# Kernel optimization log

Hardware: AMD Instinct MI355X
Metric: run time of the kernel (lower is better)

## Reference

```python
import jax, jax.numpy as jnp
import numpy as np

NUM_GRAPHS = 128
N_NODES = 50000
N_EDGES = 400000
EMB = 384
L = 5
BN_EPS = 1e-5


def _bn(h, gamma, beta):
    # training-mode BatchNorm1d over the node/edge dim (biased variance, like torch)
    m = h.mean(axis=0)
    v = h.var(axis=0)
    return gamma * (h - m) * jax.lax.rsqrt(v + BN_EPS) + beta


def setup_inputs() -> dict:
    key = jax.random.key(0)
    ks = jax.random.split(key, 16)
    batch = jnp.sort(jax.random.randint(ks[0], (N_NODES,), 0, NUM_GRAPHS))
    x = jax.random.randint(ks[1], (N_NODES, 9), 0, 64)
    edge_index = jax.random.randint(ks[2], (2, N_EDGES), 0, N_NODES)
    edge_attr = jax.random.randint(ks[3], (N_EDGES, 3), 0, 8)
    s = 0.05
    atom_emb = jax.random.normal(ks[4], (9, 64, EMB), jnp.float32) * s
    bond_emb = jax.random.normal(ks[5], (3, 8, EMB), jnp.float32) * s
    # per-layer GINE MLP params, stacked over layers
    W1 = jax.random.normal(ks[6], (L, EMB, 2 * EMB), jnp.float32) * (1.0 / np.sqrt(EMB))
    b1 = jnp.zeros((L, 2 * EMB), jnp.float32)
    g1 = jnp.ones((L, 2 * EMB), jnp.float32)
    be1 = jnp.zeros((L, 2 * EMB), jnp.float32)
    W2 = jax.random.normal(ks[7], (L, 2 * EMB, EMB), jnp.float32) * (1.0 / np.sqrt(2 * EMB))
    b2 = jnp.zeros((L, EMB), jnp.float32)
    # outer per-layer BatchNorm params
    gbn = jnp.ones((L, EMB), jnp.float32)
    bbn = jnp.zeros((L, EMB), jnp.float32)
    return {"batch": batch, "x": x, "edge_index": edge_index, "edge_attr": edge_attr,
            "atom_emb": atom_emb, "bond_emb": bond_emb,
            "W1": W1, "b1": b1, "g1": g1, "be1": be1,
            "W2": W2, "b2": b2, "gbn": gbn, "bbn": bbn}


def reference(batch, x, edge_index, edge_attr, atom_emb, bond_emb,
              W1, b1, g1, be1, W2, b2, gbn, bbn):
    # AtomEncoder / BondEncoder: sum of per-column embedding lookups
    h = atom_emb[jnp.arange(9), x].sum(axis=1)          # [N, EMB]
    e = bond_emb[jnp.arange(3), edge_attr].sum(axis=1)  # [E, EMB]
    src, dst = edge_index[0], edge_index[1]
    for i in range(W1.shape[0]):
        # GINEConv: sum_j relu(x_j + e_ij)  (edge_weight defaults to ones)
        msg = jax.nn.relu(h[src] + e)                                   # [E, EMB]
        agg = jax.ops.segment_sum(msg, dst, num_segments=N_NODES)      # [N, EMB]
        z = h + agg                                                     # (1+eps)*x_i + agg, eps=0
        # MLP: Linear -> BN -> ReLU -> Linear
        z = z @ W1[i] + b1[i]
        z = jax.nn.relu(_bn(z, g1[i], be1[i]))
        z = z @ W2[i] + b2[i]
        # outer BN + ReLU (drop_ratio = 0.0)
        h = jax.nn.relu(_bn(z, gbn[i], bbn[i]))
    # standard pooling: global_add_pool
    graph_emb = jax.ops.segment_sum(h, batch, num_segments=NUM_GRAPHS)  # [G, EMB]
    return graph_emb, h
```

## Files before the change

### kernel.cpp

```cpp
#include <hip/hip_runtime.h>
#include <stdint.h>

#define NN 50000
#define NE 400000
#define EMB 384
#define NH 768
#define NL 5

typedef __bf16 bf16x8_t __attribute__((ext_vector_type(8)));
typedef float  f32x4_t  __attribute__((ext_vector_type(4)));

__device__ __forceinline__ float bflo(uint32_t u){ union{uint32_t u;float f;} v; v.u = u<<16; return v.f; }
__device__ __forceinline__ float bfhi(uint32_t u){ union{uint32_t u;float f;} v; v.u = u & 0xffff0000u; return v.f; }
__device__ __forceinline__ uint16_t f2bf(float f){
  union{float f;uint32_t u;} v; v.f=f;
  uint32_t r = v.u + 0x7fffu + ((v.u>>16)&1u);
  return (uint16_t)(r>>16);
}
__device__ __forceinline__ uint32_t bfpack2(float a, float b){
  return (uint32_t)f2bf(a) | ((uint32_t)f2bf(b)<<16);
}

__device__ __forceinline__ void gld16(uint16_t* ldsp, const uint16_t* gp){
  __builtin_amdgcn_global_load_lds(
      (const __attribute__((address_space(1))) uint32_t*)gp,
      (__attribute__((address_space(3))) uint32_t*)ldsp,
      16, 0, 0);
}

__global__ void hist_kernel(const int* __restrict__ dst, int* __restrict__ count){
  int i = blockIdx.x*256 + threadIdx.x;
  if (i < NE) atomicAdd(&count[dst[i]], 1);
}
__global__ void scan_block_sum(const int* __restrict__ count, int* __restrict__ bsum, int n){
  __shared__ int s[256];
  int i = blockIdx.x*256 + threadIdx.x;
  s[threadIdx.x] = (i<n) ? count[i] : 0;
  __syncthreads();
  for (int st=128; st>0; st>>=1){
    if (threadIdx.x < st) s[threadIdx.x] += s[threadIdx.x+st];
    __syncthreads();
  }
  if (threadIdx.x==0) bsum[blockIdx.x] = s[0];
}
__global__ void scan_excl_small(int* __restrict__ bsum, int nb){
  __shared__ int s[256];
  int t = threadIdx.x;
  int v = (t<nb) ? bsum[t] : 0;
  s[t] = v;
  __syncthreads();
  for (int st=1; st<256; st<<=1){
    int u = (t>=st) ? s[t-st] : 0;
    __syncthreads();
    s[t] += u;
    __syncthreads();
  }
  if (t<nb) bsum[t] = s[t] - v;
}
__global__ void scan_final(const int* __restrict__ count, const int* __restrict__ bsum,
                           int* __restrict__ rowptr, int* __restrict__ cursor, int n){
  __shared__ int s[256];
  int t = threadIdx.x;
  int i = blockIdx.x*256 + t;
  int v = (i<n) ? count[i] : 0;
  s[t] = v;
  __syncthreads();
  for (int st=1; st<256; st<<=1){
    int u = (t>=st) ? s[t-st] : 0;
    __syncthreads();
    s[t] += u;
    __syncthreads();
  }
  int off = bsum[blockIdx.x] + s[t] - v;
  if (i < n){
    rowptr[i] = off; cursor[i] = off;
    if (i == n-1) rowptr[n] = off + v;
  }
}
__global__ void scatter_kernel(const int* __restrict__ dst, const int* __restrict__ src,
                               const int* __restrict__ eattr, int* __restrict__ cursor,
                               int* __restrict__ csr_src, int* __restrict__ csr_code){
  int e = blockIdx.x*256 + threadIdx.x;
  if (e < NE){
    int p = atomicAdd(&cursor[dst[e]], 1);
    csr_src[p] = src[e];
    csr_code[p] = eattr[e*3] | (eattr[e*3+1]<<3) | (eattr[e*3+2]<<6);
  }
}

__global__ void build_bond(const float* __restrict__ bemb, uint16_t* __restrict__ bt){
  const int code = blockIdx.x;
  const int t0 = code&7, t1=(code>>3)&7, t2=code>>6;
  const int c = threadIdx.x;
  const float2 a = ((const float2*)(bemb + (size_t)( 0+t0)*EMB))[c];
  const float2 b = ((const float2*)(bemb + (size_t)( 8+t1)*EMB))[c];
  const float2 d = ((const float2*)(bemb + (size_t)(16+t2)*EMB))[c];
  ((uint32_t*)(bt + (size_t)code*EMB))[c] = bfpack2(a.x+b.x+d.x, a.y+b.y+d.y);
}

__global__ void transpose_w(const float* __restrict__ in, uint16_t* __restrict__ outp,
                            int R, int Cc){
  __shared__ float tile[32][33];
  const size_t lo = (size_t)blockIdx.z * R * Cc;
  int cb = blockIdx.x*32, rb = blockIdx.y*32;
  int r = rb + threadIdx.y, c = cb + threadIdx.x;
  if (r < R && c < Cc) tile[threadIdx.y][threadIdx.x] = in[lo + (size_t)r*Cc + c];
  __syncthreads();
  int orr = cb + threadIdx.y, occ = rb + threadIdx.x;
  if (orr < Cc && occ < R) outp[lo + (size_t)orr*R + occ] = f2bf(tile[threadIdx.x][threadIdx.y]);
}

__global__ __launch_bounds__(256) void atom_encode(
    const int* __restrict__ x, const float* __restrict__ aemb,
    uint16_t* __restrict__ h){
  const int w = threadIdx.x >> 6, lane = threadIdx.x & 63;
  const int i = blockIdx.x*4 + w;
  if (i >= NN) return;
  float a0=0,a1=0,a2=0,a3=0,a4=0,a5=0;
  #pragma unroll
  for (int k=0;k<9;k++){
    const int idx = x[i*9+k];
    const float2* p = (const float2*)(aemb + ((size_t)(k*64+idx))*EMB) + lane*3;
    float2 u0=p[0], u1=p[1], u2=p[2];
    a0+=u0.x; a1+=u0.y; a2+=u1.x; a3+=u1.y; a4+=u2.x; a5+=u2.y;
  }
  uint32_t* hp = (uint32_t*)(h + (size_t)i*EMB) + lane*3;
  hp[0]=bfpack2(a0,a1); hp[1]=bfpack2(a2,a3); hp[2]=bfpack2(a4,a5);
}

template<int BNREL>
__global__ __launch_bounds__(256) void agg_kernel(
    const uint16_t* __restrict__ in, const uint16_t* __restrict__ bondt,
    const float* __restrict__ scale, const float* __restrict__ shift,
    const int* __restrict__ rowptr, const int* __restrict__ csr_src,
    const int* __restrict__ csr_code, uint16_t* __restrict__ za){
  const int w = threadIdx.x >> 6, lane = threadIdx.x & 63;
  const int i = blockIdx.x*4 + w;
  if (i >= NN) return;

  float sc0=0,sc1=0,sc2=0,sc3=0,sc4=0,sc5=0, sh0=0,sh1=0,sh2=0,sh3=0,sh4=0,sh5=0;
  if (BNREL){
    const int c = lane*6;
    sc0=scale[c]; sc1=scale[c+1]; sc2=scale[c+2]; sc3=scale[c+3]; sc4=scale[c+4]; sc5=scale[c+5];
    sh0=shift[c]; sh1=shift[c+1]; sh2=shift[c+2]; sh3=shift[c+3]; sh4=shift[c+4]; sh5=shift[c+5];
  }

  const uint32_t* hs = (const uint32_t*)(in + (size_t)i*EMB) + lane*3;
  uint32_t s0=hs[0], s1=hs[1], s2=hs[2];
  float a0,a1,a2,a3,a4,a5;
  if (BNREL){
    a0 = fmaxf(bflo(s0)*sc0+sh0, 0.f); a1 = fmaxf(bfhi(s0)*sc1+sh1, 0.f);
    a2 = fmaxf(bflo(s1)*sc2+sh2, 0.f); a3 = fmaxf(bfhi(s1)*sc3+sh3, 0.f);
    a4 = fmaxf(bflo(s2)*sc4+sh4, 0.f); a5 = fmaxf(bfhi(s2)*sc5+sh5, 0.f);
  } else {
    a0 = bflo(s0); a1 = bfhi(s0); a2 = bflo(s1); a3 = bfhi(s1); a4 = bflo(s2); a5 = bfhi(s2);
  }

  const int rs = rowptr[i], re = rowptr[i+1];
  int k = rs;
  for (; k + 4 <= re; k += 4){
    int sj[4], cj[4];
    #pragma unroll
    for (int j=0;j<4;j++){ sj[j]=csr_src[k+j]; cj[j]=csr_code[k+j]; }
    uint32_t u[4][3], b[4][3];
    #pragma unroll
    for (int j=0;j<4;j++){
      const uint32_t* hp = (const uint32_t*)(in + (size_t)sj[j]*EMB) + lane*3;
      u[j][0]=hp[0]; u[j][1]=hp[1]; u[j][2]=hp[2];
      const uint32_t* bp = (const uint32_t*)(bondt + (size_t)cj[j]*EMB) + lane*3;
      b[j][0]=bp[0]; b[j][1]=bp[1]; b[j][2]=bp[2];
    }
    #pragma unroll
    for (int j=0;j<4;j++){
      float v0,v1,v2,v3,v4,v5;
      if (BNREL){
        v0 = fmaxf(bflo(u[j][0])*sc0+sh0, 0.f); v1 = fmaxf(bfhi(u[j][0])*sc1+sh1, 0.f);
        v2 = fmaxf(bflo(u[j][1])*sc2+sh2, 0.f); v3 = fmaxf(bfhi(u[j][1])*sc3+sh3, 0.f);
        v4 = fmaxf(bflo(u[j][2])*sc4+sh4, 0.f); v5 = fmaxf(bfhi(u[j][2])*sc5+sh5, 0.f);
      } else {
        v0=bflo(u[j][0]); v1=bfhi(u[j][0]); v2=bflo(u[j][1]);
        v3=bfhi(u[j][1]); v4=bflo(u[j][2]); v5=bfhi(u[j][2]);
      }
      a0 += fmaxf(v0+bflo(b[j][0]), 0.f); a1 += fmaxf(v1+bfhi(b[j][0]), 0.f);
      a2 += fmaxf(v2+bflo(b[j][1]), 0.f); a3 += fmaxf(v3+bfhi(b[j][1]), 0.f);
      a4 += fmaxf(v4+bflo(b[j][2]), 0.f); a5 += fmaxf(v5+bfhi(b[j][2]), 0.f);
    }
  }
  for (; k < re; k++){
    const int s = csr_src[k];
    const int code = csr_code[k];
    const uint32_t* hp = (const uint32_t*)(in + (size_t)s*EMB) + lane*3;
    uint32_t u0=hp[0], u1=hp[1], u2=hp[2];
    const uint32_t* bp = (const uint32_t*)(bondt + (size_t)code*EMB) + lane*3;
    uint32_t b0=bp[0], b1=bp[1], b2=bp[2];
    float v0,v1,v2,v3,v4,v5;
    if (BNREL){
      v0 = fmaxf(bflo(u0)*sc0+sh0, 0.f); v1 = fmaxf(bfhi(u0)*sc1+sh1, 0.f);
      v2 = fmaxf(bflo(u1)*sc2+sh2, 0.f); v3 = fmaxf(bfhi(u1)*sc3+sh3, 0.f);
      v4 = fmaxf(bflo(u2)*sc4+sh4, 0.f); v5 = fmaxf(bfhi(u2)*sc5+sh5, 0.f);
    } else {
      v0=bflo(u0); v1=bfhi(u0); v2=bflo(u1); v3=bfhi(u1); v4=bflo(u2); v5=bfhi(u2);
    }
    a0 += fmaxf(v0+bflo(b0), 0.f); a1 += fmaxf(v1+bfhi(b0), 0.f);
    a2 += fmaxf(v2+bflo(b1), 0.f); a3 += fmaxf(v3+bfhi(b1), 0.f);
    a4 += fmaxf(v4+bflo(b2), 0.f); a5 += fmaxf(v5+bfhi(b2), 0.f);
  }

  uint32_t* zp = (uint32_t*)(za + (size_t)i*EMB) + lane*3;
  zp[0] = bfpack2(a0,a1);
  zp[1] = bfpack2(a2,a3);
  zp[2] = bfpack2(a4,a5);
}

template<int BNA>
__global__ __launch_bounds__(256) void gemm_bt(
    const uint16_t* __restrict__ A, const uint16_t* __restrict__ Bt,
    const float* __restrict__ bias, const float* __restrict__ scA,
    const float* __restrict__ shA, uint16_t* __restrict__ C,
    float* __restrict__ stats, int M, int N, int K, int nbr){
  __shared__ __align__(16) uint16_t As[BNA ? 2 : 3][128*32];
  __shared__ __align__(16) uint16_t Bs[3][128*32];
  __shared__ float sAs[BNA ? NH : 1];
  __shared__ float hAs[BNA ? NH : 1];
  __shared__ float csum[128];
  __shared__ float csq[128];

  const int tid = threadIdx.x;
  const int nbc = N >> 7;
  const int xcd = blockIdx.x & 7;
  const int slot = blockIdx.x >> 3;
  const int bcol = slot % nbc;
  const int brow = (slot / nbc)*8 + xcd;
  if (brow >= nbr) return;
  const int rowbase = brow << 7;

  const int lane = tid & 63;
  const int w = tid >> 6;
  const int wm = w >> 1, wn = w & 1;
  const int quad = lane >> 4, l16 = lane & 15;

  const int s0 = tid, s1 = 256 + tid;
  const int kq0 = s0 >> 7, r0 = s0 & 127;
  const int kq1 = s1 >> 7, r1 = s1 & 127;
  int gra0 = rowbase + r0; if (gra0 >= M) gra0 = M-1;
  int gra1 = rowbase + r1; if (gra1 >= M) gra1 = M-1;
  const int pb0 = bcol*128 + (r0 & 64) + ((r0 & 15) << 2) + ((r0 >> 4) & 3);
  const int pb1 = bcol*128 + (r1 & 64) + ((r1 & 15) << 2) + ((r1 >> 4) & 3);

  const uint16_t* gA0 = A + (size_t)gra0*K + kq0*8;
  const uint16_t* gA1 = A + (size_t)gra1*K + kq1*8;
  const uint16_t* gB0 = Bt + (size_t)pb0*K + kq0*8;
  const uint16_t* gB1 = Bt + (size_t)pb1*K + kq1*8;

  f32x4_t acc[4][4];
  #pragma unroll
  for (int mi=0;mi<4;mi++)
    #pragma unroll
    for (int ni=0;ni<4;ni++)
      acc[mi][ni] = (f32x4_t){0.f,0.f,0.f,0.f};

  auto stageA_bn = [&](int pi, int kk, uint4 va, uint4 vb){
    uint32_t in0[4] = {va.x,va.y,va.z,va.w};
    uint32_t in1[4] = {vb.x,vb.y,vb.z,vb.w};
    uint32_t o0[4], o1[4];
    const int kb0 = kk + kq0*8, kb1 = kk + kq1*8;
    #pragma unroll
    for (int j=0;j<4;j++){
      float x0 = fmaxf(bflo(in0[j])*sAs[kb0+2*j  ]+hAs[kb0+2*j  ], 0.f);
      float x1 = fmaxf(bfhi(in0[j])*sAs[kb0+2*j+1]+hAs[kb0+2*j+1], 0.f);
      o0[j] = bfpack2(x0,x1);
      float y0 = fmaxf(bflo(in1[j])*sAs[kb1+2*j  ]+hAs[kb1+2*j  ], 0.f);
      float y1 = fmaxf(bfhi(in1[j])*sAs[kb1+2*j+1]+hAs[kb1+2*j+1], 0.f);
      o1[j] = bfpack2(y0,y1);
    }
    *(uint4*)&As[pi][s0*8] = make_uint4(o0[0],o0[1],o0[2],o0[3]);
    *(uint4*)&As[pi][s1*8] = make_uint4(o1[0],o1[1],o1[2],o1[3]);
  };
  auto computeT = [&](int ai, int bi){
    bf16x8_t fa[4], fb[4];
    #pragma unroll
    for (int mi=0;mi<4;mi++)
      fa[mi] = *(const bf16x8_t*)&As[ai][(quad*128 + wm*64 + mi*16 + l16)*8];
    #pragma unroll
    for (int ni=0;ni<4;ni++)
      fb[ni] = *(const bf16x8_t*)&Bs[bi][(quad*128 + wn*64 + ni*16 + l16)*8];
    #pragma unroll
    for (int mi=0;mi<4;mi++)
      #pragma unroll
      for (int ni=0;ni<4;ni++)
        acc[mi][ni] = __builtin_amdgcn_mfma_f32_16x16x32_bf16(fa[mi], fb[ni], acc[mi][ni], 0,0,0);
  };

  const int nk = K >> 5;

  uint4 ar[2][2];
  if (BNA){
    for (int i = tid; i < K; i += 256){ sAs[i] = scA[i]; hAs[i] = shA[i]; }
    __syncthreads();
    ar[0][0] = *(const uint4*)(gA0);
    ar[0][1] = *(const uint4*)(gA1);
  } else {
    gld16(&As[0][s0*8], gA0);
    gld16(&As[0][s1*8], gA1);
  }
  gld16(&Bs[0][s0*8], gB0);
  gld16(&Bs[0][s1*8], gB1);
  __builtin_amdgcn_sched_barrier(0);
  if (BNA){
    ar[1][0] = *(const uint4*)(gA0 + 32);
    ar[1][1] = *(const uint4*)(gA1 + 32);
  } else {
    gld16(&As[1][s0*8], gA0 + 32);
    gld16(&As[1][s1*8], gA1 + 32);
  }
  gld16(&Bs[1][s0*8], gB0 + 32);
  gld16(&Bs[1][s1*8], gB1 + 32);

  for (int base = 0; base < nk; base += 6){
    #pragma unroll
    for (int j = 0; j < 6; j++){
      const int t = base + j;
      if (t < nk - 1) asm volatile("s_waitcnt vmcnt(4)" ::: "memory");
      else            asm volatile("s_waitcnt vmcnt(0)" ::: "memory");
      if (BNA){
        stageA_bn(j & 1, t*32, ar[j & 1][0], ar[j & 1][1]);
        asm volatile("s_waitcnt lgkmcnt(0)" ::: "memory");
      }
      __builtin_amdgcn_s_barrier();
      __builtin_amdgcn_sched_barrier(0);
      if (t + 2 < nk){
        if (BNA){
          ar[j & 1][0] = *(const uint4*)(gA0 + (t+2)*32);
          ar[j & 1][1] = *(const uint4*)(gA1 + (t+2)*32);
        } else {
          gld16(&As[(j+2)%3][s0*8], gA0 + (t+2)*32);
          gld16(&As[(j+2)%3][s1*8], gA1 + (t+2)*32);
        }
        gld16(&Bs[(j+2)%3][s0*8], gB0 + (t+2)*32);
        gld16(&Bs[(j+2)%3][s1*8], gB1 + (t+2)*32);
      }
      computeT(BNA ? (j & 1) : (j % 3), j % 3);
    }
  }

  if (tid < 128){ csum[tid]=0.f; csq[tid]=0.f; }
  __syncthreads();

  const int lcol = wn*64 + l16*4;
  const int colbase = bcol*128 + lcol;
  float bv[4], ssum[4] = {0,0,0,0}, sq[4] = {0,0,0,0};
  #pragma unroll
  for (int ni=0;ni<4;ni++) bv[ni] = bias[colbase + ni];

  #pragma unroll
  for (int mi=0;mi<4;mi++){
    #pragma unroll
    for (int r=0;r<4;r++){
      const int grow = rowbase + wm*64 + mi*16 + quad*4 + r;
      if (grow < M){
        float v0 = acc[mi][0][r] + bv[0];
        float v1 = acc[mi][1][r] + bv[1];
        float v2 = acc[mi][2][r] + bv[2];
        float v3 = acc[mi][3][r] + bv[3];
        uint2 pk = make_uint2(bfpack2(v0,v1), bfpack2(v2,v3));
        *(uint2*)(C + (size_t)grow*N + colbase) = pk;
        ssum[0]+=v0; ssum[1]+=v1; ssum[2]+=v2; ssum[3]+=v3;
        sq[0]+=v0*v0; sq[1]+=v1*v1; sq[2]+=v2*v2; sq[3]+=v3*v3;
      }
    }
  }
  #pragma unroll
  for (int ni=0;ni<4;ni++){
    ssum[ni] += __shfl_xor(ssum[ni], 16); ssum[ni] += __shfl_xor(ssum[ni], 32);
    sq[ni]   += __shfl_xor(sq[ni],   16); sq[ni]   += __shfl_xor(sq[ni],   32);
  }
  if (quad == 0){
    #pragma unroll
    for (int ni=0;ni<4;ni++){
      atomicAdd(&csum[lcol + ni], ssum[ni]);
      atomicAdd(&csq [lcol + ni], sq[ni]);
    }
  }
  __syncthreads();
  if (tid < 128){
    atomicAdd(&stats[bcol*128 + tid], csum[tid]);
    atomicAdd(&stats[N + bcol*128 + tid], csq[tid]);
  }
}

__global__ void bn_finalize(float* __restrict__ stats, const float* __restrict__ gamma,
                            const float* __restrict__ beta, float* __restrict__ scale,
                            float* __restrict__ shift, int n, float invM){
  int c = blockIdx.x*256 + threadIdx.x;
  if (c < n){
    float mean = stats[c]*invM;
    float var  = stats[n+c]*invM - mean*mean;
    float sc = gamma[c] * rsqrtf(var + 1e-5f);
    scale[c] = sc;
    shift[c] = beta[c] - mean*sc;
    stats[c] = 0.f;
    stats[n+c] = 0.f;
  }
}

__global__ void bn_relu_final(const uint16_t* __restrict__ u, const float* __restrict__ scale,
                              const float* __restrict__ shift, float* __restrict__ hf){
  int i = blockIdx.x*256 + threadIdx.x;
  const int total2 = NN*EMB/2;
  if (i >= total2) return;
  uint32_t v = ((const uint32_t*)u)[i];
  int c = (i*2) % EMB;
  float f0 = fmaxf(bflo(v)*scale[c  ] + shift[c  ], 0.f);
  float f1 = fmaxf(bfhi(v)*scale[c+1] + shift[c+1], 0.f);
  ((float2*)hf)[i] = make_float2(f0, f1);
}

__global__ void pool_kernel(const float* __restrict__ h, const int* __restrict__ batch,
                            float* __restrict__ pool){
  __shared__ int bs[64];
  int c = threadIdx.x;
  int n0 = blockIdx.x*64;
  if (c < 64){ int i = n0 + c; bs[c] = (i < NN) ? batch[i] : -1; }
  __syncthreads();
  float sum = 0.f; int cur = -1;
  for (int tt=0; tt<64; tt++){
    int i = n0 + tt;
    if (i >= NN) break;
    int g = bs[tt];
    float v = h[(size_t)i*EMB + c];
    if (g != cur){
      if (cur >= 0) atomicAdd(&pool[(size_t)cur*EMB + c], sum);
      cur = g; sum = v;
    } else sum += v;
  }
  if (cur >= 0) atomicAdd(&pool[(size_t)cur*EMB + c], sum);
}
__global__ void pool_to_out(const float* __restrict__ pool, float* __restrict__ outp){
  int i = blockIdx.x*256 + threadIdx.x;
  if (i < 128*EMB) outp[i] = pool[i];
}

extern "C" void kernel_launch(void* const* d_in, const int* in_sizes, int n_in,
                              void* d_out, int out_size, void* d_ws, size_t ws_size,
                              hipStream_t stream){
  (void)in_sizes; (void)n_in; (void)out_size; (void)ws_size;
  const int* batch = (const int*)d_in[0];
  const int* x     = (const int*)d_in[1];
  const int* eidx  = (const int*)d_in[2];
  const int* eattr = (const int*)d_in[3];
  const float* aemb = (const float*)d_in[4];
  const float* bemb = (const float*)d_in[5];
  const float* W1 = (const float*)d_in[6];
  const float* b1 = (const float*)d_in[7];
  const float* g1 = (const float*)d_in[8];
  const float* be1= (const float*)d_in[9];
  const float* W2 = (const float*)d_in[10];
  const float* b2 = (const float*)d_in[11];
  const float* gbn= (const float*)d_in[12];
  const float* bbn= (const float*)d_in[13];
  float* out = (float*)d_out;

  char* base = (char*)d_ws;
  size_t off = 0;
  auto alloc = [&](size_t bytes) -> void* {
    void* p = base + off;
    off = (off + bytes + 255) & ~(size_t)255;
    return p;
  };
  uint16_t* za   = (uint16_t*)alloc((size_t)NN*EMB*2);
  uint16_t* zm   = (uint16_t*)alloc((size_t)NN*EMB*2);
  uint16_t* t    = (uint16_t*)alloc((size_t)NN*NH*2);
  uint16_t* W1t  = (uint16_t*)alloc((size_t)NL*NH*EMB*2);
  uint16_t* W2t  = (uint16_t*)alloc((size_t)NL*EMB*NH*2);
  uint16_t* bondt= (uint16_t*)alloc((size_t)512*EMB*2);
  float* stats1  = (float*)alloc(NH*2*4);
  float* stats2  = (float*)alloc(EMB*2*4);
  float* scale1  = (float*)alloc(NH*4);
  float* shift1  = (float*)alloc(NH*4);
  float* scale2  = (float*)alloc(EMB*4);
  float* shift2  = (float*)alloc(EMB*4);
  float* pool    = (float*)alloc(128*EMB*4);
  int* count   = (int*)alloc((size_t)NN*4);
  int* rowptr  = (int*)alloc((size_t)(NN+1)*4);
  int* cursor  = (int*)alloc((size_t)NN*4);
  int* bsum    = (int*)alloc(256*4);
  int* csr_src = (int*)alloc((size_t)NE*4);
  int* csr_code= (int*)alloc((size_t)NE*4);

  const int* esrc = eidx;
  const int* edst = eidx + NE;
  const int nsb = (NN + 255)/256;

  hipMemsetAsync(count, 0, (size_t)NN*4, stream);
  hist_kernel<<<(NE+255)/256, 256, 0, stream>>>(edst, count);
  scan_block_sum<<<nsb, 256, 0, stream>>>(count, bsum, NN);
  scan_excl_small<<<1, 256, 0, stream>>>(bsum, nsb);
  scan_final<<<nsb, 256, 0, stream>>>(count, bsum, rowptr, cursor, NN);
  scatter_kernel<<<(NE+255)/256, 256, 0, stream>>>(edst, esrc, eattr, cursor, csr_src, csr_code);

  build_bond<<<512, 192, 0, stream>>>(bemb, bondt);
  transpose_w<<<dim3(NH/32, EMB/32, NL), dim3(32,32), 0, stream>>>(W1, W1t, EMB, NH);
  transpose_w<<<dim3(EMB/32, NH/32, NL), dim3(32,32), 0, stream>>>(W2, W2t, NH, EMB);

  atom_encode<<<NN/4, 256, 0, stream>>>(x, aemb, zm);
  hipMemsetAsync(pool, 0, (size_t)128*EMB*4, stream);
  hipMemsetAsync(stats1, 0, (size_t)(6144 + 3072), stream);

  const int nbr = (NN + 127)/128;
  const int nbrr = ((nbr + 7)/8)*8;
  const int g1blocks = nbrr*(NH/128);
  const int g2blocks = nbrr*(EMB/128);
  for (int l = 0; l < NL; l++){
    if (l == 0)
      agg_kernel<0><<<NN/4, 256, 0, stream>>>(zm, bondt, nullptr, nullptr,
                                              rowptr, csr_src, csr_code, za);
    else
      agg_kernel<1><<<NN/4, 256, 0, stream>>>(zm, bondt, scale2, shift2,
                                              rowptr, csr_src, csr_code, za);
    gemm_bt<0><<<g1blocks, 256, 0, stream>>>(
        za, W1t + (size_t)l*NH*EMB, b1 + l*NH, nullptr, nullptr, t, stats1, NN, NH, EMB, nbr);
    bn_finalize<<<(NH+255)/256, 256, 0, stream>>>(stats1, g1 + l*NH, be1 + l*NH,
                                                  scale1, shift1, NH, 1.0f/NN);
    gemm_bt<1><<<g2blocks, 256, 0, stream>>>(
        t, W2t + (size_t)l*EMB*NH, b2 + l*EMB, scale1, shift1, zm, stats2, NN, EMB, NH, nbr);
    bn_finalize<<<(EMB+255)/256, 256, 0, stream>>>(stats2, gbn + l*EMB, bbn + l*EMB,
                                                   scale2, shift2, EMB, 1.0f/NN);
  }
  bn_relu_final<<<(NN*EMB/2 + 255)/256, 256, 0, stream>>>(zm, scale2, shift2, out + 128*EMB);
  pool_kernel<<<(NN+63)/64, 384, 0, stream>>>(out + 128*EMB, batch, pool);
  pool_to_out<<<(128*EMB+255)/256, 256, 0, stream>>>(pool, out);
}
```

Measured before the change: 1.332 ms.

## Restructure BN-fused GEMM into single-buffer register-prefetch pipeline with hardware bf16 pack

For the BN-applied A-operand GEMM variant, the triple-buffered LDS pipeline built on direct global-to-LDS loads is replaced with a single LDS buffer per operand. Both A and B tiles are now prefetched into registers two k-steps ahead and stored to LDS, with __syncthreads around each compute step. The aim is to cut LDS use (for higher occupancy) and simplify synchronisation for that variant. Separately, the software round-to-nearest bf16 packing is swapped for the v_cvt_pk_bf16_f32 instruction in the BN staging and the epilogue. This trades the async LDS-load overlap for two full barriers per k-step and more register pressure.

```diff
diff --git a/kernel.cpp b/kernel.cpp
--- a/kernel.cpp
+++ b/kernel.cpp
@@ -19,6 +19,11 @@
 }
 __device__ __forceinline__ uint32_t bfpack2(float a, float b){
   return (uint32_t)f2bf(a) | ((uint32_t)f2bf(b)<<16);
+}
+__device__ __forceinline__ uint32_t bfpack2h(float a, float b){
+  uint32_t r;
+  asm("v_cvt_pk_bf16_f32 %0, %1, %2" : "=v"(r) : "v"(a), "v"(b));
+  return r;
 }
 
 __device__ __forceinline__ void gld16(uint16_t* ldsp, const uint16_t* gp){
@@ -218,8 +223,8 @@
     const float* __restrict__ bias, const float* __restrict__ scA,
     const float* __restrict__ shA, uint16_t* __restrict__ C,
     float* __restrict__ stats, int M, int N, int K, int nbr){
-  __shared__ __align__(16) uint16_t As[BNA ? 2 : 3][128*32];
-  __shared__ __align__(16) uint16_t Bs[3][128*32];
+  __shared__ __align__(16) uint16_t As[BNA ? 1 : 3][128*32];
+  __shared__ __align__(16) uint16_t Bs[BNA ? 1 : 3][128*32];
   __shared__ float sAs[BNA ? NH : 1];
   __shared__ float hAs[BNA ? NH : 1];
   __shared__ float csum[128];
@@ -259,7 +264,7 @@
     for (int ni=0;ni<4;ni++)
       acc[mi][ni] = (f32x4_t){0.f,0.f,0.f,0.f};
 
-  auto stageA_bn = [&](int pi, int kk, uint4 va, uint4 vb){
+  auto stageA_bn = [&](int kk, uint4 va, uint4 vb){
     uint32_t in0[4] = {va.x,va.y,va.z,va.w};
     uint32_t in1[4] = {vb.x,vb.y,vb.z,vb.w};
     uint32_t o0[4], o1[4];
@@ -268,13 +273,13 @@
     for (int j=0;j<4;j++){
       float x0 = fmaxf(bflo(in0[j])*sAs[kb0+2*j  ]+hAs[kb0+2*j  ], 0.f);
       float x1 = fmaxf(bfhi(in0[j])*sAs[kb0+2*j+1]+hAs[kb0+2*j+1], 0.f);
-      o0[j] = bfpack2(x0,x1);
+      o0[j] = bfpack2h(x0,x1);
       float y0 = fmaxf(bflo(in1[j])*sAs[kb1+2*j  ]+hAs[kb1+2*j  ], 0.f);
       float y1 = fmaxf(bfhi(in1[j])*sAs[kb1+2*j+1]+hAs[kb1+2*j+1], 0.f);
-      o1[j] = bfpack2(y0,y1);
-    }
-    *(uint4*)&As[pi][s0*8] = make_uint4(o0[0],o0[1],o0[2],o0[3]);
-    *(uint4*)&As[pi][s1*8] = make_uint4(o1[0],o1[1],o1[2],o1[3]);
+      o1[j] = bfpack2h(y0,y1);
+    }
+    *(uint4*)&As[0][s0*8] = make_uint4(o0[0],o0[1],o0[2],o0[3]);
+    *(uint4*)&As[0][s1*8] = make_uint4(o1[0],o1[1],o1[2],o1[3]);
   };
   auto computeT = [&](int ai, int bi){
     bf16x8_t fa[4], fb[4];
@@ -293,53 +298,75 @@
 
   const int nk = K >> 5;
 
-  uint4 ar[2][2];
   if (BNA){
+    uint4 pa0 = *(const uint4*)gA0;
+    uint4 pa1 = *(const uint4*)gA1;
+    uint4 pb0r = *(const uint4*)gB0;
+    uint4 pb1r = *(const uint4*)gB1;
+    uint4 qa0 = *(const uint4*)(gA0 + 32);
+    uint4 qa1 = *(const uint4*)(gA1 + 32);
+    uint4 qb0r = *(const uint4*)(gB0 + 32);
+    uint4 qb1r = *(const uint4*)(gB1 + 32);
+
     for (int i = tid; i < K; i += 256){ sAs[i] = scA[i]; hAs[i] = shA[i]; }
     __syncthreads();
-    ar[0][0] = *(const uint4*)(gA0);
-    ar[0][1] = *(const uint4*)(gA1);
+
+    for (int k0 = 0; k0 < K; k0 += 64){
+      stageA_bn(k0, pa0, pa1);
+      *(uint4*)&Bs[0][s0*8] = pb0r;
+      *(uint4*)&Bs[0][s1*8] = pb1r;
+      __syncthreads();
+      if (k0 + 64 < K){
+        const int kn = k0 + 64;
+        pa0 = *(const uint4*)(gA0 + kn);
+        pa1 = *(const uint4*)(gA1 + kn);
+        pb0r = *(const uint4*)(gB0 + kn);
+        pb1r = *(const uint4*)(gB1 + kn);
+      }
+      computeT(0, 0);
+      __syncthreads();
+
+      stageA_bn(k0 + 32, qa0, qa1);
+      *(uint4*)&Bs[0][s0*8] = qb0r;
+      *(uint4*)&Bs[0][s1*8] = qb1r;
+      __syncthreads();
+      if (k0 + 96 < K){
+        const int kn = k0 + 96;
+        qa0 = *(const uint4*)(gA0 + kn);
+        qa1 = *(const uint4*)(gA1 + kn);
+        qb0r = *(const uint4*)(gB0 + kn);
+        qb1r = *(const uint4*)(gB1 + kn);
+      }
+      computeT(0, 0);
+      __syncthreads();
+    }
   } else {
     gld16(&As[0][s0*8], gA0);
     gld16(&As[0][s1*8], gA1);
-  }
-  gld16(&Bs[0][s0*8], gB0);
-  gld16(&Bs[0][s1*8], gB1);
-  __builtin_amdgcn_sched_barrier(0);
-  if (BNA){
-    ar[1][0] = *(const uint4*)(gA0 + 32);
-    ar[1][1] = *(const uint4*)(gA1 + 32);
-  } else {
+    gld16(&Bs[0][s0*8], gB0);
+    gld16(&Bs[0][s1*8], gB1);
+    __builtin_amdgcn_sched_barrier(0);
     gld16(&As[1][s0*8], gA0 + 32);
     gld16(&As[1][s1*8], gA1 + 32);
-  }
-  gld16(&Bs[1][s0*8], gB0 + 32);
-  gld16(&Bs[1][s1*8], gB1 + 32);
-
-  for (int base = 0; base < nk; base += 6){
-    #pragma unroll
-    for (int j = 0; j < 6; j++){
-      const int t = base + j;
-      if (t < nk - 1) asm volatile("s_waitcnt vmcnt(4)" ::: "memory");
-      else            asm volatile("s_waitcnt vmcnt(0)" ::: "memory");
-      if (BNA){
-        stageA_bn(j & 1, t*32, ar[j & 1][0], ar[j & 1][1]);
-        asm volatile("s_waitcnt lgkmcnt(0)" ::: "memory");
-      }
-      __builtin_amdgcn_s_barrier();
-      __builtin_amdgcn_sched_barrier(0);
-      if (t + 2 < nk){
-        if (BNA){
-          ar[j & 1][0] = *(const uint4*)(gA0 + (t+2)*32);
-          ar[j & 1][1] = *(const uint4*)(gA1 + (t+2)*32);
-        } else {
+    gld16(&Bs[1][s0*8], gB0 + 32);
+    gld16(&Bs[1][s1*8], gB1 + 32);
+
+    for (int base = 0; base < nk; base += 6){
+      #pragma unroll
+      for (int j = 0; j < 6; j++){
+        const int t = base + j;
+        if (t < nk - 1) asm volatile("s_waitcnt vmcnt(4)" ::: "memory");
+        else            asm volatile("s_waitcnt vmcnt(0)" ::: "memory");
+        __builtin_amdgcn_s_barrier();
+        __builtin_amdgcn_sched_barrier(0);
+        if (t + 2 < nk){
           gld16(&As[(j+2)%3][s0*8], gA0 + (t+2)*32);
           gld16(&As[(j+2)%3][s1*8], gA1 + (t+2)*32);
+          gld16(&Bs[(j+2)%3][s0*8], gB0 + (t+2)*32);
+          gld16(&Bs[(j+2)%3][s1*8], gB1 + (t+2)*32);
         }
-        gld16(&Bs[(j+2)%3][s0*8], gB0 + (t+2)*32);
-        gld16(&Bs[(j+2)%3][s1*8], gB1 + (t+2)*32);
+        computeT(j % 3, j % 3);
       }
-      computeT(BNA ? (j & 1) : (j % 3), j % 3);
     }
   }
 
@@ -362,7 +389,7 @@
         float v1 = acc[mi][1][r] + bv[1];
         float v2 = acc[mi][2][r] + bv[2];
         float v3 = acc[mi][3][r] + bv[3];
-        uint2 pk = make_uint2(bfpack2(v0,v1), bfpack2(v2,v3));
+        uint2 pk = make_uint2(bfpack2h(v0,v1), bfpack2h(v2,v3));
         *(uint2*)(C + (size_t)grow*N + colbase) = pk;
         ssum[0]+=v0; ssum[1]+=v1; ssum[2]+=v2; ssum[3]+=v3;
         sq[0]+=v0*v0; sq[1]+=v1*v1; sq[2]+=v2*v2; sq[3]+=v3*v3;
```

After: 1.283 ms. 3.7% less time.

## Restructure GEMM to load B panels into LDS and stream A directly into registers

Applied to the files above, without the earlier changes.

The tiled GEMM used a triple-buffered LDS pipeline for both A and B. It now loads a 192-wide K panel of B into LDS once per part, and each wave reads its own 32 rows of A from global memory straight into MFMA operand registers, applying the BN+ReLU prologue there. This removes the A-tile LDS traffic and the per-k-step barriers, leaving one barrier pair per panel. It also switches to the hardware packed bf16 convert and sets occupancy hints through launch bounds. The cost is loads that no longer overlap across panels and less reuse of A across waves, since each wave covers all 128 columns.

```diff
diff --git a/kernel.cpp b/kernel.cpp
--- a/kernel.cpp
+++ b/kernel.cpp
@@ -19,6 +19,14 @@
 }
 __device__ __forceinline__ uint32_t bfpack2(float a, float b){
   return (uint32_t)f2bf(a) | ((uint32_t)f2bf(b)<<16);
+}
+__device__ __forceinline__ uint32_t bfpack2h(float a, float b){
+  uint32_t r;
+  asm("v_cvt_pk_bf16_f32 %0, %1, %2" : "=v"(r) : "v"(a), "v"(b));
+  return r;
+}
+__device__ __forceinline__ bf16x8_t as_bf16x8(uint4 u){
+  union{uint4 a; bf16x8_t b;} c; c.a = u; return c.b;
 }
 
 __device__ __forceinline__ void gld16(uint16_t* ldsp, const uint16_t* gp){
@@ -212,16 +220,16 @@
   zp[2] = bfpack2(a4,a5);
 }
 
-template<int BNA>
-__global__ __launch_bounds__(256) void gemm_bt(
+template<int BNA, int KK>
+__global__ __launch_bounds__(256, BNA ? 2 : 3) void gemm_bt(
     const uint16_t* __restrict__ A, const uint16_t* __restrict__ Bt,
     const float* __restrict__ bias, const float* __restrict__ scA,
     const float* __restrict__ shA, uint16_t* __restrict__ C,
-    float* __restrict__ stats, int M, int N, int K, int nbr){
-  __shared__ __align__(16) uint16_t As[BNA ? 2 : 3][128*32];
-  __shared__ __align__(16) uint16_t Bs[3][128*32];
-  __shared__ float sAs[BNA ? NH : 1];
-  __shared__ float hAs[BNA ? NH : 1];
+    float* __restrict__ stats, int M, int N, int nbr){
+  constexpr int NPART = KK / 192;
+  __shared__ __align__(16) uint16_t panel[6*4096];
+  __shared__ float sAs[BNA ? KK : 1];
+  __shared__ float hAs[BNA ? KK : 1];
   __shared__ float csum[128];
   __shared__ float csq[128];
 
@@ -236,150 +244,134 @@
 
   const int lane = tid & 63;
   const int w = tid >> 6;
-  const int wm = w >> 1, wn = w & 1;
   const int quad = lane >> 4, l16 = lane & 15;
 
   const int s0 = tid, s1 = 256 + tid;
-  const int kq0 = s0 >> 7, r0 = s0 & 127;
-  const int kq1 = s1 >> 7, r1 = s1 & 127;
-  int gra0 = rowbase + r0; if (gra0 >= M) gra0 = M-1;
-  int gra1 = rowbase + r1; if (gra1 >= M) gra1 = M-1;
+  const int r0 = s0 & 127, r1 = s1 & 127;
   const int pb0 = bcol*128 + (r0 & 64) + ((r0 & 15) << 2) + ((r0 >> 4) & 3);
   const int pb1 = bcol*128 + (r1 & 64) + ((r1 & 15) << 2) + ((r1 >> 4) & 3);
-
-  const uint16_t* gA0 = A + (size_t)gra0*K + kq0*8;
-  const uint16_t* gA1 = A + (size_t)gra1*K + kq1*8;
-  const uint16_t* gB0 = Bt + (size_t)pb0*K + kq0*8;
-  const uint16_t* gB1 = Bt + (size_t)pb1*K + kq1*8;
-
-  f32x4_t acc[4][4];
+  const uint16_t* gB0 = Bt + (size_t)pb0*KK + (s0>>7)*8;
+  const uint16_t* gB1 = Bt + (size_t)pb1*KK + (s1>>7)*8;
+
+  int rowA0 = rowbase + w*32 + l16;      if (rowA0 >= M) rowA0 = M-1;
+  int rowA1 = rowbase + w*32 + 16 + l16; if (rowA1 >= M) rowA1 = M-1;
+  const uint16_t* gA0 = A + (size_t)rowA0*KK + quad*8;
+  const uint16_t* gA1 = A + (size_t)rowA1*KK + quad*8;
+
+  if (BNA){
+    for (int i = tid; i < KK; i += 256){ sAs[i] = scA[i]; hAs[i] = shA[i]; }
+  }
+
+  f32x4_t acc[2][2][4];
   #pragma unroll
-  for (int mi=0;mi<4;mi++)
-    #pragma unroll
-    for (int ni=0;ni<4;ni++)
-      acc[mi][ni] = (f32x4_t){0.f,0.f,0.f,0.f};
-
-  auto stageA_bn = [&](int pi, int kk, uint4 va, uint4 vb){
-    uint32_t in0[4] = {va.x,va.y,va.z,va.w};
-    uint32_t in1[4] = {vb.x,vb.y,vb.z,vb.w};
-    uint32_t o0[4], o1[4];
-    const int kb0 = kk + kq0*8, kb1 = kk + kq1*8;
-    #pragma unroll
-    for (int j=0;j<4;j++){
-      float x0 = fmaxf(bflo(in0[j])*sAs[kb0+2*j  ]+hAs[kb0+2*j  ], 0.f);
-      float x1 = fmaxf(bfhi(in0[j])*sAs[kb0+2*j+1]+hAs[kb0+2*j+1], 0.f);
-      o0[j] = bfpack2(x0,x1);
-      float y0 = fmaxf(bflo(in1[j])*sAs[kb1+2*j  ]+hAs[kb1+2*j  ], 0.f);
-      float y1 = fmaxf(bfhi(in1[j])*sAs[kb1+2*j+1]+hAs[kb1+2*j+1], 0.f);
-      o1[j] = bfpack2(y0,y1);
-    }
-    *(uint4*)&As[pi][s0*8] = make_uint4(o0[0],o0[1],o0[2],o0[3]);
-    *(uint4*)&As[pi][s1*8] = make_uint4(o1[0],o1[1],o1[2],o1[3]);
-  };
-  auto computeT = [&](int ai, int bi){
-    bf16x8_t fa[4], fb[4];
-    #pragma unroll
-    for (int mi=0;mi<4;mi++)
-      fa[mi] = *(const bf16x8_t*)&As[ai][(quad*128 + wm*64 + mi*16 + l16)*8];
-    #pragma unroll
-    for (int ni=0;ni<4;ni++)
-      fb[ni] = *(const bf16x8_t*)&Bs[bi][(quad*128 + wn*64 + ni*16 + l16)*8];
-    #pragma unroll
-    for (int mi=0;mi<4;mi++)
+  for (int mi=0;mi<2;mi++)
+    #pragma unroll
+    for (int g=0;g<2;g++)
       #pragma unroll
-      for (int ni=0;ni<4;ni++)
-        acc[mi][ni] = __builtin_amdgcn_mfma_f32_16x16x32_bf16(fa[mi], fb[ni], acc[mi][ni], 0,0,0);
-  };
-
-  const int nk = K >> 5;
-
-  uint4 ar[2][2];
-  if (BNA){
-    for (int i = tid; i < K; i += 256){ sAs[i] = scA[i]; hAs[i] = shA[i]; }
+      for (int nj=0;nj<4;nj++)
+        acc[mi][g][nj] = (f32x4_t){0.f,0.f,0.f,0.f};
+
+  for (int part = 0; part < NPART; ++part){
+    const int k0 = part*192;
+    if (part) __syncthreads();
+    #pragma unroll
+    for (int sl = 0; sl < 6; ++sl){
+      gld16(&panel[sl*4096 + s0*8], gB0 + k0 + sl*32);
+      gld16(&panel[sl*4096 + s1*8], gB1 + k0 + sl*32);
+    }
+    uint4 ca0 = *(const uint4*)(gA0 + k0);
+    uint4 ca1 = *(const uint4*)(gA1 + k0);
     __syncthreads();
-    ar[0][0] = *(const uint4*)(gA0);
-    ar[0][1] = *(const uint4*)(gA1);
-  } else {
-    gld16(&As[0][s0*8], gA0);
-    gld16(&As[0][s1*8], gA1);
-  }
-  gld16(&Bs[0][s0*8], gB0);
-  gld16(&Bs[0][s1*8], gB1);
-  __builtin_amdgcn_sched_barrier(0);
-  if (BNA){
-    ar[1][0] = *(const uint4*)(gA0 + 32);
-    ar[1][1] = *(const uint4*)(gA1 + 32);
-  } else {
-    gld16(&As[1][s0*8], gA0 + 32);
-    gld16(&As[1][s1*8], gA1 + 32);
-  }
-  gld16(&Bs[1][s0*8], gB0 + 32);
-  gld16(&Bs[1][s1*8], gB1 + 32);
-
-  for (int base = 0; base < nk; base += 6){
-    #pragma unroll
-    for (int j = 0; j < 6; j++){
-      const int t = base + j;
-      if (t < nk - 1) asm volatile("s_waitcnt vmcnt(4)" ::: "memory");
-      else            asm volatile("s_waitcnt vmcnt(0)" ::: "memory");
+
+    uint4 na0, na1;
+    #pragma unroll
+    for (int kq = 0; kq < 6; ++kq){
+      if (kq < 5){
+        na0 = *(const uint4*)(gA0 + k0 + (kq+1)*32);
+        na1 = *(const uint4*)(gA1 + k0 + (kq+1)*32);
+      }
+      bf16x8_t fa0, fa1;
       if (BNA){
-        stageA_bn(j & 1, t*32, ar[j & 1][0], ar[j & 1][1]);
-        asm volatile("s_waitcnt lgkmcnt(0)" ::: "memory");
+        const int kb = k0 + kq*32 + quad*8;
+        float4 sv0 = *(const float4*)&sAs[kb];
+        float4 sv1 = *(const float4*)&sAs[kb+4];
+        float4 hv0 = *(const float4*)&hAs[kb];
+        float4 hv1 = *(const float4*)&hAs[kb+4];
+        float e0,e1,e2,e3,e4,e5,e6,e7;
+        e0=fmaxf(bflo(ca0.x)*sv0.x+hv0.x,0.f); e1=fmaxf(bfhi(ca0.x)*sv0.y+hv0.y,0.f);
+        e2=fmaxf(bflo(ca0.y)*sv0.z+hv0.z,0.f); e3=fmaxf(bfhi(ca0.y)*sv0.w+hv0.w,0.f);
+        e4=fmaxf(bflo(ca0.z)*sv1.x+hv1.x,0.f); e5=fmaxf(bfhi(ca0.z)*sv1.y+hv1.y,0.f);
+        e6=fmaxf(bflo(ca0.w)*sv1.z+hv1.z,0.f); e7=fmaxf(bfhi(ca0.w)*sv1.w+hv1.w,0.f);
+        fa0 = as_bf16x8(make_uint4(bfpack2h(e0,e1),bfpack2h(e2,e3),bfpack2h(e4,e5),bfpack2h(e6,e7)));
+        e0=fmaxf(bflo(ca1.x)*sv0.x+hv0.x,0.f); e1=fmaxf(bfhi(ca1.x)*sv0.y+hv0.y,0.f);
+        e2=fmaxf(bflo(ca1.y)*sv0.z+hv0.z,0.f); e3=fmaxf(bfhi(ca1.y)*sv0.w+hv0.w,0.f);
+        e4=fmaxf(bflo(ca1.z)*sv1.x+hv1.x,0.f); e5=fmaxf(bfhi(ca1.z)*sv1.y+hv1.y,0.f);
+        e6=fmaxf(bflo(ca1.w)*sv1.z+hv1.z,0.f); e7=fmaxf(bfhi(ca1.w)*sv1.w+hv1.w,0.f);
+        fa1 = as_bf16x8(make_uint4(bfpack2h(e0,e1),bfpack2h(e2,e3),bfpack2h(e4,e5),bfpack2h(e6,e7)));
+      } else {
+        fa0 = as_bf16x8(ca0);
+        fa1 = as_bf16x8(ca1);
       }
-      __builtin_amdgcn_s_barrier();
-      __builtin_amdgcn_sched_barrier(0);
-      if (t + 2 < nk){
-        if (BNA){
-          ar[j & 1][0] = *(const uint4*)(gA0 + (t+2)*32);
-          ar[j & 1][1] = *(const uint4*)(gA1 + (t+2)*32);
-        } else {
-          gld16(&As[(j+2)%3][s0*8], gA0 + (t+2)*32);
-          gld16(&As[(j+2)%3][s1*8], gA1 + (t+2)*32);
+      #pragma unroll
+      for (int g=0; g<2; ++g)
+        #pragma unroll
+        for (int nj=0; nj<4; ++nj){
+          bf16x8_t fb = *(const bf16x8_t*)&panel[kq*4096 + (quad*128 + g*64 + nj*16 + l16)*8];
+          acc[0][g][nj] = __builtin_amdgcn_mfma_f32_16x16x32_bf16(fa0, fb, acc[0][g][nj], 0,0,0);
+          acc[1][g][nj] = __builtin_amdgcn_mfma_f32_16x16x32_bf16(fa1, fb, acc[1][g][nj], 0,0,0);
         }
-        gld16(&Bs[(j+2)%3][s0*8], gB0 + (t+2)*32);
-        gld16(&Bs[(j+2)%3][s1*8], gB1 + (t+2)*32);
+      ca0 = na0; ca1 = na1;
+    }
+  }
+
+  if (tid < 128){ csum[tid]=0.f; csq[tid]=0.f; }
+  __syncthreads();
+
+  const int colbase = bcol*128 + l16*4;
+  float bv[2][4], ssum[2][4], sq[2][4];
+  #pragma unroll
+  for (int g=0;g<2;g++)
+    #pragma unroll
+    for (int nj=0;nj<4;nj++){
+      bv[g][nj] = bias[colbase + g*64 + nj];
+      ssum[g][nj] = 0.f; sq[g][nj] = 0.f;
+    }
+
+  #pragma unroll
+  for (int mi=0;mi<2;mi++){
+    #pragma unroll
+    for (int r=0;r<4;r++){
+      const int grow = rowbase + w*32 + mi*16 + quad*4 + r;
+      if (grow < M){
+        #pragma unroll
+        for (int g=0;g<2;g++){
+          float v0 = acc[mi][g][0][r] + bv[g][0];
+          float v1 = acc[mi][g][1][r] + bv[g][1];
+          float v2 = acc[mi][g][2][r] + bv[g][2];
+          float v3 = acc[mi][g][3][r] + bv[g][3];
+          uint2 pk = make_uint2(bfpack2h(v0,v1), bfpack2h(v2,v3));
+          *(uint2*)(C + (size_t)grow*N + colbase + g*64) = pk;
+          ssum[g][0]+=v0; ssum[g][1]+=v1; ssum[g][2]+=v2; ssum[g][3]+=v3;
+          sq[g][0]+=v0*v0; sq[g][1]+=v1*v1; sq[g][2]+=v2*v2; sq[g][3]+=v3*v3;
+        }
       }
-      computeT(BNA ? (j & 1) : (j % 3), j % 3);
-    }
-  }
-
-  if (tid < 128){ csum[tid]=0.f; csq[tid]=0.f; }
-  __syncthreads();
-
-  const int lcol = wn*64 + l16*4;
-  const int colbase = bcol*128 + lcol;
-  float bv[4], ssum[4] = {0,0,0,0}, sq[4] = {0,0,0,0};
+    }
+  }
   #pragma unroll
-  for (int ni=0;ni<4;ni++) bv[ni] = bias[colbase + ni];
-
-  #pragma unroll
-  for (int mi=0;mi<4;mi++){
-    #pragma unroll
-    for (int r=0;r<4;r++){
-      const int grow = rowbase + wm*64 + mi*16 + quad*4 + r;
-      if (grow < M){
-        float v0 = acc[mi][0][r] + bv[0];
-        float v1 = acc[mi][1][r] + bv[1];
-        float v2 = acc[mi][2][r] + bv[2];
-        float v3 = acc[mi][3][r] + bv[3];
-        uint2 pk = make_uint2(bfpack2(v0,v1), bfpack2(v2,v3));
-        *(uint2*)(C + (size_t)grow*N + colbase) = pk;
-        ssum[0]+=v0; ssum[1]+=v1; ssum[2]+=v2; ssum[3]+=v3;
-        sq[0]+=v0*v0; sq[1]+=v1*v1; sq[2]+=v2*v2; sq[3]+=v3*v3;
+  for (int g=0;g<2;g++)
+    #pragma unroll
+    for (int nj=0;nj<4;nj++){
+      ssum[g][nj] += __shfl_xor(ssum[g][nj], 16); ssum[g][nj] += __shfl_xor(ssum[g][nj], 32);
+      sq[g][nj]   += __shfl_xor(sq[g][nj],   16); sq[g][nj]   += __shfl_xor(sq[g][nj],   32);
+    }
+  if (quad == 0){
+    #pragma unroll
+    for (int g=0;g<2;g++)
+      #pragma unroll
+      for (int nj=0;nj<4;nj++){
+        atomicAdd(&csum[g*64 + l16*4 + nj], ssum[g][nj]);
+        atomicAdd(&csq [g*64 + l16*4 + nj], sq[g][nj]);
       }
-    }
-  }
-  #pragma unroll
-  for (int ni=0;ni<4;ni++){
-    ssum[ni] += __shfl_xor(ssum[ni], 16); ssum[ni] += __shfl_xor(ssum[ni], 32);
-    sq[ni]   += __shfl_xor(sq[ni],   16); sq[ni]   += __shfl_xor(sq[ni],   32);
-  }
-  if (quad == 0){
-    #pragma unroll
-    for (int ni=0;ni<4;ni++){
-      atomicAdd(&csum[lcol + ni], ssum[ni]);
-      atomicAdd(&csq [lcol + ni], sq[ni]);
-    }
   }
   __syncthreads();
   if (tid < 128){
@@ -517,12 +509,12 @@
     else
       agg_kernel<1><<<NN/4, 256, 0, stream>>>(zm, bondt, scale2, shift2,
                                               rowptr, csr_src, csr_code, za);
-    gemm_bt<0><<<g1blocks, 256, 0, stream>>>(
-        za, W1t + (size_t)l*NH*EMB, b1 + l*NH, nullptr, nullptr, t, stats1, NN, NH, EMB, nbr);
+    gemm_bt<0, EMB><<<g1blocks, 256, 0, stream>>>(
+        za, W1t + (size_t)l*NH*EMB, b1 + l*NH, nullptr, nullptr, t, stats1, NN, NH, nbr);
     bn_finalize<<<(NH+255)/256, 256, 0, stream>>>(stats1, g1 + l*NH, be1 + l*NH,
                                                   scale1, shift1, NH, 1.0f/NN);
-    gemm_bt<1><<<g2blocks, 256, 0, stream>>>(
-        t, W2t + (size_t)l*EMB*NH, b2 + l*EMB, scale1, shift1, zm, stats2, NN, EMB, NH, nbr);
+    gemm_bt<1, NH><<<g2blocks, 256, 0, stream>>>(
+        t, W2t + (size_t)l*EMB*NH, b2 + l*EMB, scale1, shift1, zm, stats2, NN, EMB, nbr);
     bn_finalize<<<(EMB+255)/256, 256, 0, stream>>>(stats2, gbn + l*EMB, bbn + l*EMB,
                                                    scale2, shift2, EMB, 1.0f/NN);
   }
```

After: 1.354 ms. Within noise of the previous version (+1.7%).
